# Kernel optimization log

Measured on AMD Instinct MI355X. Metric: run time of the kernel, lower is better.

The kernel has to match this reference:

```python
import jax, jax.numpy as jnp
import numpy as np

# Config (matches init_kwargs)
B, T_IN, N, F_IN = 64, 12, 500, 2
N_RES, N_DIL, N_SKIP, N_END = 64, 64, 256, 512
K_SIZE, N_BLOCKS, N_LAYERS = 2, 4, 2
EDGE_DIM, N_PRED, N_OUT = 2, 12, 1
RECEPTIVE = N_BLOCKS * (K_SIZE - 1) * (2 ** N_LAYERS - 1) + 1  # 13
DILS = [2 ** i for _ in range(N_BLOCKS) for i in range(N_LAYERS)]  # [1,2,1,2,1,2,1,2]
L = len(DILS)
BN_EPS = 1e-5


def setup_inputs() -> dict:
    key = jax.random.key(0)
    ks = jax.random.split(key, 20)
    inputs = jax.random.normal(ks[0], (B, T_IN, N, F_IN), dtype=jnp.float32)
    u = jax.random.uniform(ks[1], (EDGE_DIM, N, N), dtype=jnp.float32)
    supports = u / u.sum(-1, keepdims=True)  # row-stochastic diffusion matrices
    def w(k, shape, fan_in):
        return jax.random.normal(k, shape, dtype=jnp.float32) * (1.0 / np.sqrt(fan_in))
    return {
        "inputs": inputs,
        "supports": supports,
        "enter_w": w(ks[2], (N_RES, F_IN), F_IN),
        "enter_b": jnp.zeros((N_RES,), jnp.float32),
        "filter_w": w(ks[3], (L, N_DIL, N_RES, 1, K_SIZE), N_RES * K_SIZE),
        "filter_b": jnp.zeros((L, N_DIL), jnp.float32),
        "gate_w": w(ks[4], (L, N_DIL, N_RES, 1, K_SIZE), N_RES * K_SIZE),
        "gate_b": jnp.zeros((L, N_DIL), jnp.float32),
        "gconv_w": w(ks[5], (L, N_RES, EDGE_DIM * N_DIL), EDGE_DIM * N_DIL),
        "gconv_b": jnp.zeros((L, N_RES), jnp.float32),
        "skip_w": w(ks[6], (L, N_SKIP, N_DIL), N_DIL),
        "skip_b": jnp.zeros((L, N_SKIP), jnp.float32),
        "bn_gamma": jnp.ones((L, N_RES), jnp.float32),
        "bn_beta": jnp.zeros((L, N_RES), jnp.float32),
        "out1_w": w(ks[7], (N_END, N_SKIP), N_SKIP),
        "out1_b": jnp.zeros((N_END,), jnp.float32),
        "out2_w": w(ks[8], (N_PRED * N_OUT, N_END), N_END),
        "out2_b": jnp.zeros((N_PRED * N_OUT,), jnp.float32),
    }


def _conv_t(x, w, b, dil):
    # x: [B,C,N,T], w: [O,I,1,k] dilated along time, VALID padding
    y = jax.lax.conv_general_dilated(x, w, window_strides=(1, 1), padding="VALID",
                                     rhs_dilation=(1, dil),
                                     dimension_numbers=("NCHW", "OIHW", "NCHW"))
    return y + b[None, :, None, None]


def _forward(inputs, supports, enter_w, enter_b, filter_w, filter_b, gate_w, gate_b,
             gconv_w, gconv_b, skip_w, skip_b, bn_gamma, bn_beta,
             out1_w, out1_b, out2_w, out2_b):
    x = jnp.transpose(inputs, (0, 3, 2, 1))  # [B,F,N,T]
    pad = RECEPTIVE - x.shape[3]
    if pad > 0:
        x = jnp.pad(x, ((0, 0), (0, 0), (0, 0), (pad, 0)))
    x = jnp.einsum("of,bfnt->bont", enter_w, x) + enter_b[None, :, None, None]
    b = x.shape[0]
    skip = jnp.zeros((b, N_SKIP, N, x.shape[3]), jnp.float32)
    for i, d in enumerate(DILS):
        residual = x
        f = jnp.tanh(_conv_t(residual, filter_w[i], filter_b[i], d))
        g = jax.nn.sigmoid(_conv_t(residual, gate_w[i], gate_b[i], d))
        x = f * g  # [B, n_dil, N, t']
        s = jnp.einsum("oc,bcnt->bont", skip_w[i], x) + skip_b[i][None, :, None, None]
        skip = skip[..., -s.shape[3]:] + s
        # graph diffusion conv: propagate over each support, mix channels
        h = jnp.einsum("knm,bcmt->bkcnt", supports, x)
        bb, kk, cc, nn, tt = h.shape
        h = h.reshape(bb, kk * cc, nn, tt)
        x = jnp.einsum("oi,bint->bont", gconv_w[i], h) + gconv_b[i][None, :, None, None]
        # dropout is identity in eval mode
        x = x + residual[..., -x.shape[3]:]
        # BatchNorm2d (training-mode batch statistics)
        mean = x.mean(axis=(0, 2, 3), keepdims=True)
        var = ((x - mean) ** 2).mean(axis=(0, 2, 3), keepdims=True)
        x = (x - mean) * jax.lax.rsqrt(var + BN_EPS)
        x = x * bn_gamma[i][None, :, None, None] + bn_beta[i][None, :, None, None]
    y = jax.nn.relu(skip)  # [B, n_skips, N, 1]
    y = jax.nn.relu(jnp.einsum("os,bsnt->bont", out1_w, y) + out1_b[None, :, None, None])
    y = jnp.einsum("oe,bent->bont", out2_w, y) + out2_b[None, :, None, None]
    # [B, n_pred*n_out, N, 1] -> [B, n_pred, N, n_out]
    y = y.reshape(b, N_PRED, -1, N)
    return jnp.swapaxes(y, -1, -2)


def reference(inputs, supports, enter_w, enter_b, filter_w, filter_b, gate_w, gate_b,
              gconv_w, gconv_b, skip_w, skip_b, bn_gamma, bn_beta,
              out1_w, out1_b, out2_w, out2_b):
    return _forward(inputs, supports, enter_w, enter_b, filter_w, filter_b, gate_w, gate_b,
                    gconv_w, gconv_b, skip_w, skip_b, bn_gamma, bn_beta,
                    out1_w, out1_b, out2_w, out2_b)
```

## Files before the change

### kernel.cpp

```cpp
#include <hip/hip_runtime.h>

typedef float v4 __attribute__((ext_vector_type(4)));
typedef short bf8 __attribute__((ext_vector_type(8)));
typedef unsigned short u16;
typedef unsigned int u32;

#define DEVI __device__ __forceinline__

namespace {

constexpr int B = 64, C = 64, NPT = 500, NP = 512, T0 = 13, SC = 256, EC = 512, PR = 12;
constexpr size_t SLOTP = (size_t)B * C * NP;

constexpr size_t SZ_BUF  = 13 * SLOTP * 2;
constexpr size_t OFF_SK  = 2 * SZ_BUF;
constexpr size_t SZ_SK   = (size_t)SC * B * NPT * 4;
constexpr size_t OFF_ST  = OFF_SK + SZ_SK;
constexpr size_t OFF_STP = OFF_ST + 1024;
constexpr size_t OFF_W1T = OFF_STP + 1024;
constexpr size_t OFF_WMX = OFF_W1T + (size_t)131072*4;
constexpr size_t OFF_WFB = OFF_WMX + (size_t)65536*2;
constexpr size_t OFF_WGB = OFF_WFB + (size_t)65536*2;
constexpr size_t OFF_SWB = OFF_WGB + (size_t)65536*2;
constexpr size_t OFF_SPD = OFF_SWB + (size_t)131072*2;
constexpr size_t WS_NEED = OFF_SPD + (size_t)524288*2;

DEVI float sigm(float x) { return 1.f / (1.f + expf(-x)); }
DEVI float bf2f(u16 u) { u32 x = ((u32)u) << 16; float f; __builtin_memcpy(&f, &x, 4); return f; }
DEVI u16 f2bf(float f) { u32 x; __builtin_memcpy(&x, &f, 4); return (u16)((x + 0x7FFF + ((x >> 16) & 1)) >> 16); }
DEVI int swzA(int n, int k) { int byte = (n << 8) + (k << 1); byte ^= (((n >> 1) ^ (n >> 3)) & 7) << 4; return byte; }
DEVI int swzS(int n, int cp) { int byte = (n << 7) + (cp << 1); byte ^= (((n >> 1) ^ (n >> 3)) & 7) << 4; return byte; }

__global__ void k_debug_ws(float* __restrict__ out, float val) {
  int i = blockIdx.x * 256 + threadIdx.x;
  if (i < B * PR * NPT) out[i] = val;
}

__global__ void k_prep(const float* __restrict__ fw, const float* __restrict__ gw,
                       const float* __restrict__ sw, const float* __restrict__ gcw,
                       const float* __restrict__ o1w, const float* __restrict__ sup,
                       u16* __restrict__ WFB, u16* __restrict__ WGB,
                       u16* __restrict__ SWB, u16* __restrict__ WMX,
                       float* __restrict__ W1T, u16* __restrict__ SPD,
                       float* __restrict__ STP, double* __restrict__ ST) {
  int i = blockIdx.x * 256 + threadIdx.x;
  if (i < 65536) {
    int k = i & 127, cp = (i >> 7) & 63, l = i >> 13;
    int tap = k >> 6, c = k & 63;
    int g = ((l * 64 + cp) * 64 + c) * 2 + tap;
    WFB[i] = f2bf(fw[g]);
    WGB[i] = f2bf(gw[g]);
  }
  int j = i - 65536;
  if (j >= 0 && j < 131072) {
    int c = j & 63, o = (j >> 6) & 255, l = j >> 14;
    SWB[j] = f2bf(sw[(l * 256 + o) * 64 + c]);
  }
  int k2 = i - 196608;
  if (k2 >= 0 && k2 < 65536) WMX[k2] = f2bf(gcw[k2]);
  int m = i - 262144;
  if (m >= 0 && m < 131072) {
    int e = m & 511, o = m >> 9;
    W1T[m] = o1w[e * 256 + o];
  }
  int sp = i - 393216;
  if (sp >= 0 && sp < 524288) {
    int mm = sp & 511, n = (sp >> 9) & 511, s = sp >> 18;
    float v = (n < NPT && mm < NPT) ? sup[(size_t)s * NPT * NPT + (size_t)n * NPT + mm] : 0.f;
    SPD[sp] = f2bf(v);
  }
  int q = i - 917504;
  if (q >= 0 && q < 192) STP[q] = (q >= 64 && q < 128) ? 1.f : 0.f;
  int z = i - 917696;
  if (z >= 0 && z < 128) ST[z] = 0.0;
}

__global__ void k_enter(const float* __restrict__ in, const float* __restrict__ ew,
                        const float* __restrict__ eb, u16* __restrict__ X) {
  size_t idx = (size_t)blockIdx.x * 256 + threadIdx.x;
  if (idx >= 13 * SLOTP) return;
  int t = (int)(idx / SLOTP);
  size_t r = idx % SLOTP;
  int n = (int)(r % NP);
  int c = (int)((r / NP) % C);
  int b = (int)(r / ((size_t)NP * C));
  float v = 0.f;
  if (n < NPT) {
    v = eb[c];
    if (t > 0) {
      const float* ip = in + (((size_t)b * 12 + (t - 1)) * NPT + n) * 2;
      v += ew[c * 2] * ip[0] + ew[c * 2 + 1] * ip[1];
    }
  }
  X[idx] = f2bf(v);
}

__global__ void k_zero_sk(float* __restrict__ p) {
  size_t i = ((size_t)blockIdx.x * 256 + threadIdx.x) * 4;
  v4 z = {};
  *(v4*)&p[i] = z;
}

__global__ __launch_bounds__(512) void k_gatedconv(
    const u16* __restrict__ X, u16* __restrict__ XA,
    const float* __restrict__ STP,
    const u16* __restrict__ WFl, const float* __restrict__ bfb,
    const u16* __restrict__ WGl, const float* __restrict__ bgb,
    const u16* __restrict__ SWl, const float* __restrict__ sb,
    float* __restrict__ SK, int d, int Tp) {
  __shared__ u16 L[65536];
  const int lane = threadIdx.x, w = threadIdx.y;
  const int tid = w * 64 + lane;
  const int t = blockIdx.x, b = blockIdx.y;
  const int lrow = lane & 15, kgrp = lane >> 4;
  const int nbase = w * 64;

  for (int i = tid; i < 8192; i += 512) {
    int tap = i >> 12;
    int c = (i >> 6) & 63;
    int n0 = (i & 63) * 8;
    const u16* src = &X[(size_t)(t + tap * d) * SLOTP + ((size_t)b * C + c) * NP + n0];
    float mean = STP[c], scl = STP[64 + c], sh = STP[128 + c];
    ushort4 a = *(const ushort4*)src;
    ushort4 a2 = *(const ushort4*)(src + 4);
    u16 vals[8] = {a.x, a.y, a.z, a.w, a2.x, a2.y, a2.z, a2.w};
    int k = tap * 64 + c;
#pragma unroll
    for (int jj = 0; jj < 8; ++jj) {
      int n = n0 + jj;
      L[swzA(n, k) >> 1] = f2bf((bf2f(vals[jj]) - mean) * scl + sh);
    }
  }
  __syncthreads();

  v4 af[4][4], ag[4][4];
#pragma unroll
  for (int a1 = 0; a1 < 4; ++a1)
#pragma unroll
    for (int a2 = 0; a2 < 4; ++a2) { af[a1][a2] = (v4){0.f,0.f,0.f,0.f}; ag[a1][a2] = (v4){0.f,0.f,0.f,0.f}; }

#pragma unroll
  for (int k0 = 0; k0 < 128; k0 += 32) {
    const int kof = k0 + kgrp * 8;
    bf8 Av[4];
#pragma unroll
    for (int nt = 0; nt < 4; ++nt) {
      int n = nbase + nt * 16 + lrow;
      Av[nt] = *(const bf8*)&L[swzA(n, kof) >> 1];
    }
#pragma unroll
    for (int ct = 0; ct < 4; ++ct) {
      bf8 Fw = *(const bf8*)&WFl[(size_t)(ct * 16 + lrow) * 128 + kof];
      bf8 Gw = *(const bf8*)&WGl[(size_t)(ct * 16 + lrow) * 128 + kof];
#pragma unroll
      for (int nt = 0; nt < 4; ++nt) {
        af[nt][ct] = __builtin_amdgcn_mfma_f32_16x16x32_bf16(Av[nt], Fw, af[nt][ct], 0, 0, 0);
        ag[nt][ct] = __builtin_amdgcn_mfma_f32_16x16x32_bf16(Av[nt], Gw, ag[nt][ct], 0, 0, 0);
      }
    }
  }

  const size_t xab = (size_t)t * SLOTP + (size_t)b * C * NP;
  ushort4 ovv[4][4];
#pragma unroll
  for (int nt = 0; nt < 4; ++nt) {
    int n0s = nbase + nt * 16 + kgrp * 4;
#pragma unroll
    for (int ct = 0; ct < 4; ++ct) {
      int cp = ct * 16 + lrow;
      float fb = bfb[cp], gb2 = bgb[cp];
      ushort4 ov;
      ov.x = f2bf(tanhf(af[nt][ct][0] + fb) * sigm(ag[nt][ct][0] + gb2));
      ov.y = f2bf(tanhf(af[nt][ct][1] + fb) * sigm(ag[nt][ct][1] + gb2));
      ov.z = f2bf(tanhf(af[nt][ct][2] + fb) * sigm(ag[nt][ct][2] + gb2));
      ov.w = f2bf(tanhf(af[nt][ct][3] + fb) * sigm(ag[nt][ct][3] + gb2));
      ovv[nt][ct] = ov;
      if (n0s < NPT) *(ushort4*)&XA[xab + (size_t)cp * NP + n0s] = ov;
    }
  }

  if (t == Tp - 1) {
    __syncthreads();
#pragma unroll
    for (int nt = 0; nt < 4; ++nt) {
      int n0s = nbase + nt * 16 + kgrp * 4;
#pragma unroll
      for (int ct = 0; ct < 4; ++ct) {
        int cp = ct * 16 + lrow;
        ushort4 ov = ovv[nt][ct];
        L[swzS(n0s + 0, cp) >> 1] = ov.x;
        L[swzS(n0s + 1, cp) >> 1] = ov.y;
        L[swzS(n0s + 2, cp) >> 1] = ov.z;
        L[swzS(n0s + 3, cp) >> 1] = ov.w;
      }
    }
    __syncthreads();
#pragma unroll 1
    for (int ot = 0; ot < 16; ++ot) {
      v4 a[4];
#pragma unroll
      for (int nt = 0; nt < 4; ++nt) a[nt] = (v4){0.f,0.f,0.f,0.f};
#pragma unroll
      for (int k0 = 0; k0 < 64; k0 += 32) {
        const int kof = k0 + kgrp * 8;
        bf8 Bs = *(const bf8*)&SWl[(size_t)(ot * 16 + lrow) * 64 + kof];
#pragma unroll
        for (int nt = 0; nt < 4; ++nt) {
          int n = nbase + nt * 16 + lrow;
          bf8 Av2 = *(const bf8*)&L[swzS(n, kof) >> 1];
          a[nt] = __builtin_amdgcn_mfma_f32_16x16x32_bf16(Av2, Bs, a[nt], 0, 0, 0);
        }
      }
      int o = ot * 16 + lrow;
      float bb = sb[o];
#pragma unroll
      for (int nt = 0; nt < 4; ++nt) {
        int n0s = nbase + nt * 16 + kgrp * 4;
        if (n0s < NPT) {
          float* dst = &SK[(size_t)o * (B * NPT) + (size_t)b * NPT + n0s];
          v4 old = *(const v4*)dst;
          *(v4*)dst = old + a[nt] + bb;
        }
      }
    }
  }
}

__global__ __launch_bounds__(512) void k_diffmix(
    const u16* __restrict__ XA, const u16* __restrict__ XIN, u16* __restrict__ XOUT,
    const u16* __restrict__ SPD, const u16* __restrict__ WMXl,
    const float* __restrict__ gb, const float* __restrict__ STP, int d) {
  __shared__ u16 G[512 * 128];
  const int lane = threadIdx.x;
  const int w = threadIdx.y;
  const int t = blockIdx.x, b = blockIdx.y;
  const int lrow = lane & 15;
  const int kgrp = lane >> 4;
  const int nbase = w * 64;
  const size_t xabase = ((size_t)t * (B * C) + (size_t)b * C) * NP;

#pragma unroll 1
  for (int s = 0; s < 2; ++s) {
    v4 acc[4][4];
#pragma unroll
    for (int a = 0; a < 4; ++a)
#pragma unroll
      for (int c2 = 0; c2 < 4; ++c2) acc[a][c2] = (v4){0.f, 0.f, 0.f, 0.f};
    const u16* Sb = SPD + (size_t)s * (512 * 512);
#pragma unroll 2
    for (int k0 = 0; k0 < 512; k0 += 32) {
      const int kof = k0 + kgrp * 8;
      bf8 Af[4], Bf[4];
#pragma unroll
      for (int nt = 0; nt < 4; ++nt)
        Af[nt] = *(const bf8*)&Sb[(size_t)(nbase + nt * 16 + lrow) * 512 + kof];
#pragma unroll
      for (int ct = 0; ct < 4; ++ct)
        Bf[ct] = *(const bf8*)&XA[xabase + (size_t)(ct * 16 + lrow) * NP + kof];
#pragma unroll
      for (int nt = 0; nt < 4; ++nt)
#pragma unroll
        for (int ct = 0; ct < 4; ++ct)
          acc[nt][ct] = __builtin_amdgcn_mfma_f32_16x16x32_bf16(Af[nt], Bf[ct], acc[nt][ct], 0, 0, 0);
    }
#pragma unroll
    for (int nt = 0; nt < 4; ++nt)
#pragma unroll
      for (int ct = 0; ct < 4; ++ct)
#pragma unroll
        for (int r = 0; r < 4; ++r) {
          int n = nbase + nt * 16 + kgrp * 4 + r;
          int k = s * 64 + ct * 16 + lrow;
          int byte = (n << 8) + (k << 1);
          byte ^= (n & 7) << 4;
          G[byte >> 1] = f2bf(acc[nt][ct][r]);
        }
  }
  __syncthreads();
  v4 acc2[4][4];
#pragma unroll
  for (int a = 0; a < 4; ++a)
#pragma unroll
    for (int c2 = 0; c2 < 4; ++c2) acc2[a][c2] = (v4){0.f, 0.f, 0.f, 0.f};
#pragma unroll
  for (int k0 = 0; k0 < 128; k0 += 32) {
    const int kof = k0 + kgrp * 8;
    bf8 Af[4], Bf[4];
#pragma unroll
    for (int nt = 0; nt < 4; ++nt) {
      int n = nbase + nt * 16 + lrow;
      int byte = (n << 8) + (kof << 1);
      byte ^= (n & 7) << 4;
      Af[nt] = *(const bf8*)&G[byte >> 1];
    }
#pragma unroll
    for (int ot = 0; ot < 4; ++ot)
      Bf[ot] = *(const bf8*)&WMXl[(size_t)(ot * 16 + lrow) * 128 + kof];
#pragma unroll
    for (int nt = 0; nt < 4; ++nt)
#pragma unroll
      for (int ot = 0; ot < 4; ++ot)
        acc2[nt][ot] = __builtin_amdgcn_mfma_f32_16x16x32_bf16(Af[nt], Bf[ot], acc2[nt][ot], 0, 0, 0);
  }
  const size_t rbase = ((size_t)(t + d) * (B * C) + (size_t)b * C) * NP;
#pragma unroll
  for (int nt = 0; nt < 4; ++nt) {
    int n0 = nbase + nt * 16 + kgrp * 4;
    if (n0 >= NPT) continue;
#pragma unroll
    for (int ot = 0; ot < 4; ++ot) {
      int o = ot * 16 + lrow;
      float bias = gb[o];
      float m = STP[o], s2 = STP[64 + o], h = STP[128 + o];
      ushort4 rv = *(const ushort4*)&XIN[rbase + (size_t)o * NP + n0];
      ushort4 ov;
      ov.x = f2bf(acc2[nt][ot][0] + bias + (bf2f(rv.x) - m) * s2 + h);
      ov.y = f2bf(acc2[nt][ot][1] + bias + (bf2f(rv.y) - m) * s2 + h);
      ov.z = f2bf(acc2[nt][ot][2] + bias + (bf2f(rv.z) - m) * s2 + h);
      ov.w = f2bf(acc2[nt][ot][3] + bias + (bf2f(rv.w) - m) * s2 + h);
      *(ushort4*)&XOUT[xabase + (size_t)o * NP + n0] = ov;
    }
  }
}

__global__ void k_bnstats(const u16* __restrict__ X, double* __restrict__ st, int Tp) {
  int c = blockIdx.y;
  int perv = Tp * B * 125;
  double s = 0.0, ss = 0.0;
  for (int p = blockIdx.x * 256 + threadIdx.x; p < perv; p += 8 * 256) {
    int t = p / (B * 125);
    int r = p - t * (B * 125);
    int b = r / 125, nv = r - b * 125;
    ushort4 u = *(const ushort4*)&X[(size_t)t * SLOTP + ((size_t)b * C + c) * NP + nv * 4];
    double x0 = (double)bf2f(u.x), x1 = (double)bf2f(u.y);
    double x2 = (double)bf2f(u.z), x3 = (double)bf2f(u.w);
    s += (x0 + x1) + (x2 + x3);
    ss += (x0 * x0 + x1 * x1) + (x2 * x2 + x3 * x3);
  }
  for (int off = 32; off; off >>= 1) {
    s += __shfl_down(s, off, 64);
    ss += __shfl_down(ss, off, 64);
  }
  if ((threadIdx.x & 63) == 0) {
    atomicAdd(&st[c], s);
    atomicAdd(&st[C + c], ss);
  }
}

__global__ void k_bnfin(double* __restrict__ st, float* __restrict__ stp,
                        const float* __restrict__ gamma, const float* __restrict__ beta, int Tp) {
  int c = threadIdx.x;
  if (c < C) {
    double cnt = (double)Tp * (double)(B * NPT);
    double m = st[c] / cnt;
    double v = st[C + c] / cnt - m * m;
    stp[c] = (float)m;
    stp[C + c] = gamma[c] * rsqrtf((float)v + 1e-5f);
    stp[2 * C + c] = beta[c];
    st[c] = 0.0;
    st[C + c] = 0.0;
  }
}

__global__ __launch_bounds__(256) void k_out1(const float* __restrict__ SK,
                                              const float* __restrict__ W1T,
                                              const float* __restrict__ b1,
                                              u16* __restrict__ H1) {
  __shared__ __align__(16) float ssm[32 * 64];
  __shared__ __align__(16) float wsm[32 * 64];
  const int tx = threadIdx.x, ty = threadIdx.y;
  const int tid = ty * 16 + tx;
  const int p0 = blockIdx.x * 64, e0 = blockIdx.y * 64;
  v4 acc[4] = {};
  for (int o0 = 0; o0 < SC; o0 += 32) {
    __syncthreads();
    for (int i = tid; i < 2048; i += 256) {
      int pp = i & 63, kk = i >> 6;
      ssm[i] = fmaxf(SK[(size_t)(o0 + kk) * (B * NPT) + p0 + pp], 0.f);
      wsm[i] = W1T[(size_t)(o0 + kk) * 512 + e0 + pp];
    }
    __syncthreads();
#pragma unroll
    for (int kk = 0; kk < 32; ++kk) {
      v4 sv = *(const v4*)&ssm[kk * 64 + tx * 4];
      v4 wv = *(const v4*)&wsm[kk * 64 + ty * 4];
#pragma unroll
      for (int r = 0; r < 4; ++r) acc[r] += wv[r] * sv;
    }
  }
#pragma unroll
  for (int r = 0; r < 4; ++r) {
    int e = e0 + ty * 4 + r;
    float bb = b1[e];
    size_t ob = (size_t)e * (B * NPT) + p0 + tx * 4;
#pragma unroll
    for (int q = 0; q < 4; ++q) H1[ob + q] = f2bf(fmaxf(acc[r][q] + bb, 0.f));
  }
}

__global__ __launch_bounds__(256) void k_out2(const u16* __restrict__ H1,
                                              const float* __restrict__ W2,
                                              const float* __restrict__ b2,
                                              float* __restrict__ out) {
  int idx = blockIdx.x * 256 + threadIdx.x;
  if (idx >= B * PR * NPT) return;
  int n = idx % NPT;
  int p12 = (idx / NPT) % PR;
  int b = idx / (NPT * PR);
  size_t p = (size_t)b * NPT + n;
  const float* w = W2 + p12 * EC;
  float acc = b2[p12];
  for (int e = 0; e < EC; e += 4) {
    acc += w[e] * bf2f(H1[(size_t)e * (B * NPT) + p])
         + w[e + 1] * bf2f(H1[(size_t)(e + 1) * (B * NPT) + p])
         + w[e + 2] * bf2f(H1[(size_t)(e + 2) * (B * NPT) + p])
         + w[e + 3] * bf2f(H1[(size_t)(e + 3) * (B * NPT) + p]);
  }
  out[idx] = acc;
}

}

extern "C" void kernel_launch(void* const* d_in, const int* in_sizes, int n_in,
                              void* d_out, int out_size, void* d_ws, size_t ws_size,
                              hipStream_t stream) {
  const float* inputs  = (const float*)d_in[0];
  const float* sup     = (const float*)d_in[1];
  const float* enter_w = (const float*)d_in[2];
  const float* enter_b = (const float*)d_in[3];
  const float* filt_w  = (const float*)d_in[4];
  const float* filt_b  = (const float*)d_in[5];
  const float* gate_w  = (const float*)d_in[6];
  const float* gate_b  = (const float*)d_in[7];
  const float* gconv_w = (const float*)d_in[8];
  const float* gconv_b = (const float*)d_in[9];
  const float* skip_w  = (const float*)d_in[10];
  const float* skip_b  = (const float*)d_in[11];
  const float* bn_g    = (const float*)d_in[12];
  const float* bn_b    = (const float*)d_in[13];
  const float* o1w     = (const float*)d_in[14];
  const float* o1b     = (const float*)d_in[15];
  const float* o2w     = (const float*)d_in[16];
  const float* o2b     = (const float*)d_in[17];
  (void)in_sizes; (void)n_in; (void)out_size;

  if (ws_size < WS_NEED) {
    k_debug_ws<<<1500, 256, 0, stream>>>((float*)d_out, (float)(ws_size >> 20));
    return;
  }

  char* base = (char*)d_ws;
  u16*    buf0 = (u16*)base;
  u16*    buf1 = (u16*)(base + SZ_BUF);
  float*  SK   = (float*)(base + OFF_SK);
  double* ST   = (double*)(base + OFF_ST);
  float*  STP  = (float*)(base + OFF_STP);
  float*  W1T  = (float*)(base + OFF_W1T);
  u16*    WMX  = (u16*)(base + OFF_WMX);
  u16*    WFB  = (u16*)(base + OFF_WFB);
  u16*    WGB  = (u16*)(base + OFF_WGB);
  u16*    SWB  = (u16*)(base + OFF_SWB);
  u16*    SPD  = (u16*)(base + OFF_SPD);

  k_prep<<<3586, 256, 0, stream>>>(filt_w, gate_w, skip_w, gconv_w, o1w, sup,
                                   WFB, WGB, SWB, WMX, W1T, SPD, STP, ST);
  k_enter<<<(int)((13 * SLOTP) / 256), 256, 0, stream>>>(inputs, enter_w, enter_b, buf0);
  k_zero_sk<<<8000, 256, 0, stream>>>(SK);

  static const int dils[8] = {1, 2, 1, 2, 1, 2, 1, 2};
  u16* bufs[2] = {buf0, buf1};
  int T = T0;
  for (int l = 0; l < 8; ++l) {
    const int d = dils[l];
    const int Tp = T - d;
    u16* XIN = bufs[l & 1];
    u16* XAb = bufs[(l + 1) & 1];
    k_gatedconv<<<dim3(Tp, B), dim3(64, 8), 0, stream>>>(
        XIN, XAb, STP, WFB + l * 8192, filt_b + l * 64, WGB + l * 8192, gate_b + l * 64,
        SWB + l * 16384, skip_b + l * 256, SK, d, Tp);
    if (l < 7) {
      k_diffmix<<<dim3(Tp, B), dim3(64, 8), 0, stream>>>(
          XAb, XIN, XAb, SPD, WMX + l * 8192, gconv_b + l * 64, STP, d);
      k_bnstats<<<dim3(8, C), 256, 0, stream>>>(XAb, ST, Tp);
      k_bnfin<<<1, 64, 0, stream>>>(ST, STP, bn_g + l * 64, bn_b + l * 64, Tp);
    }
    T = Tp;
  }

  u16* H1 = buf1;
  k_out1<<<dim3(500, 8), dim3(16, 16), 0, stream>>>(SK, W1T, o1b, H1);
  k_out2<<<1500, 256, 0, stream>>>(H1, o2w, o2b, (float*)d_out);
}
```

Before: 2.313 ms.

## Fuse BatchNorm statistics into diffusion-mix epilogue via per-block partial sums

New measurement: 3.134 ms. 35.5% more time.

```diff
diff --git a/kernel.cpp b/kernel.cpp
--- a/kernel.cpp
+++ b/kernel.cpp
@@ -23,7 +23,8 @@
 constexpr size_t OFF_WGB = OFF_WFB + (size_t)65536*2;
 constexpr size_t OFF_SWB = OFF_WGB + (size_t)65536*2;
 constexpr size_t OFF_SPD = OFF_SWB + (size_t)131072*2;
-constexpr size_t WS_NEED = OFF_SPD + (size_t)524288*2;
+constexpr size_t OFF_PSUM = OFF_SPD + (size_t)524288*2;
+constexpr size_t WS_NEED = OFF_PSUM + (size_t)768*128*4;
 
 DEVI float sigm(float x) { return 1.f / (1.f + expf(-x)); }
 DEVI float bf2f(u16 u) { u32 x = ((u32)u) << 16; float f; __builtin_memcpy(&f, &x, 4); return f; }
@@ -42,7 +43,7 @@
                        u16* __restrict__ WFB, u16* __restrict__ WGB,
                        u16* __restrict__ SWB, u16* __restrict__ WMX,
                        float* __restrict__ W1T, u16* __restrict__ SPD,
-                       float* __restrict__ STP, double* __restrict__ ST) {
+                       float* __restrict__ STP) {
   int i = blockIdx.x * 256 + threadIdx.x;
   if (i < 65536) {
     int k = i & 127, cp = (i >> 7) & 63, l = i >> 13;
@@ -71,8 +72,6 @@
   }
   int q = i - 917504;
   if (q >= 0 && q < 192) STP[q] = (q >= 64 && q < 128) ? 1.f : 0.f;
-  int z = i - 917696;
-  if (z >= 0 && z < 128) ST[z] = 0.0;
 }
 
 __global__ void k_enter(const float* __restrict__ in, const float* __restrict__ ew,
@@ -229,15 +228,19 @@
 __global__ __launch_bounds__(512) void k_diffmix(
     const u16* __restrict__ XA, const u16* __restrict__ XIN, u16* __restrict__ XOUT,
     const u16* __restrict__ SPD, const u16* __restrict__ WMXl,
-    const float* __restrict__ gb, const float* __restrict__ STP, int d) {
+    const float* __restrict__ gb, const float* __restrict__ STP,
+    float* __restrict__ PSUM, int d) {
   __shared__ u16 G[512 * 128];
+  __shared__ float sst[128];
   const int lane = threadIdx.x;
   const int w = threadIdx.y;
+  const int tid = w * 64 + lane;
   const int t = blockIdx.x, b = blockIdx.y;
   const int lrow = lane & 15;
   const int kgrp = lane >> 4;
   const int nbase = w * 64;
   const size_t xabase = ((size_t)t * (B * C) + (size_t)b * C) * NP;
+  if (tid < 128) sst[tid] = 0.f;
 
 #pragma unroll 1
   for (int s = 0; s < 2; ++s) {
@@ -302,63 +305,83 @@
       for (int ot = 0; ot < 4; ++ot)
         acc2[nt][ot] = __builtin_amdgcn_mfma_f32_16x16x32_bf16(Af[nt], Bf[ot], acc2[nt][ot], 0, 0, 0);
   }
-  const size_t rbase = ((size_t)(t + d) * (B * C) + (size_t)b * C) * NP;
+
+  __syncthreads();
 #pragma unroll
   for (int nt = 0; nt < 4; ++nt) {
     int n0 = nbase + nt * 16 + kgrp * 4;
-    if (n0 >= NPT) continue;
 #pragma unroll
     for (int ot = 0; ot < 4; ++ot) {
       int o = ot * 16 + lrow;
-      float bias = gb[o];
-      float m = STP[o], s2 = STP[64 + o], h = STP[128 + o];
-      ushort4 rv = *(const ushort4*)&XIN[rbase + (size_t)o * NP + n0];
-      ushort4 ov;
-      ov.x = f2bf(acc2[nt][ot][0] + bias + (bf2f(rv.x) - m) * s2 + h);
-      ov.y = f2bf(acc2[nt][ot][1] + bias + (bf2f(rv.y) - m) * s2 + h);
-      ov.z = f2bf(acc2[nt][ot][2] + bias + (bf2f(rv.z) - m) * s2 + h);
-      ov.w = f2bf(acc2[nt][ot][3] + bias + (bf2f(rv.w) - m) * s2 + h);
-      *(ushort4*)&XOUT[xabase + (size_t)o * NP + n0] = ov;
-    }
-  }
-}
-
-__global__ void k_bnstats(const u16* __restrict__ X, double* __restrict__ st, int Tp) {
-  int c = blockIdx.y;
-  int perv = Tp * B * 125;
-  double s = 0.0, ss = 0.0;
-  for (int p = blockIdx.x * 256 + threadIdx.x; p < perv; p += 8 * 256) {
-    int t = p / (B * 125);
-    int r = p - t * (B * 125);
-    int b = r / 125, nv = r - b * 125;
-    ushort4 u = *(const ushort4*)&X[(size_t)t * SLOTP + ((size_t)b * C + c) * NP + nv * 4];
-    double x0 = (double)bf2f(u.x), x1 = (double)bf2f(u.y);
-    double x2 = (double)bf2f(u.z), x3 = (double)bf2f(u.w);
-    s += (x0 + x1) + (x2 + x3);
-    ss += (x0 * x0 + x1 * x1) + (x2 * x2 + x3 * x3);
-  }
-  for (int off = 32; off; off >>= 1) {
-    s += __shfl_down(s, off, 64);
-    ss += __shfl_down(ss, off, 64);
-  }
-  if ((threadIdx.x & 63) == 0) {
-    atomicAdd(&st[c], s);
-    atomicAdd(&st[C + c], ss);
-  }
-}
-
-__global__ void k_bnfin(double* __restrict__ st, float* __restrict__ stp,
-                        const float* __restrict__ gamma, const float* __restrict__ beta, int Tp) {
+      int byte = (o << 10) + (n0 << 1);
+      byte ^= (o & 7) << 4;
+      ushort4 gv;
+      gv.x = f2bf(acc2[nt][ot][0]);
+      gv.y = f2bf(acc2[nt][ot][1]);
+      gv.z = f2bf(acc2[nt][ot][2]);
+      gv.w = f2bf(acc2[nt][ot][3]);
+      *(ushort4*)&G[byte >> 1] = gv;
+    }
+  }
+  __syncthreads();
+  const size_t rbase = ((size_t)(t + d) * (B * C) + (size_t)b * C) * NP;
+#pragma unroll 1
+  for (int i = 0; i < 8; ++i) {
+    int idx = i * 512 + tid;
+    int o = idx >> 6;
+    int ck = idx & 63;
+    int byte = (o << 10) + (ck << 4);
+    byte ^= (o & 7) << 4;
+    ushort4 g0 = *(const ushort4*)&G[byte >> 1];
+    ushort4 g1 = *(const ushort4*)&G[(byte >> 1) + 4];
+    int n0 = ck * 8;
+    const u16* rp = &XIN[rbase + (size_t)o * NP + n0];
+    ushort4 r0 = *(const ushort4*)rp;
+    ushort4 r1 = *(const ushort4*)(rp + 4);
+    float m = STP[o], sc = STP[64 + o], h = STP[128 + o];
+    float bias = gb[o];
+    float v[8];
+    v[0] = bf2f(g0.x) + bias + (bf2f(r0.x) - m) * sc + h;
+    v[1] = bf2f(g0.y) + bias + (bf2f(r0.y) - m) * sc + h;
+    v[2] = bf2f(g0.z) + bias + (bf2f(r0.z) - m) * sc + h;
+    v[3] = bf2f(g0.w) + bias + (bf2f(r0.w) - m) * sc + h;
+    v[4] = bf2f(g1.x) + bias + (bf2f(r1.x) - m) * sc + h;
+    v[5] = bf2f(g1.y) + bias + (bf2f(r1.y) - m) * sc + h;
+    v[6] = bf2f(g1.z) + bias + (bf2f(r1.z) - m) * sc + h;
+    v[7] = bf2f(g1.w) + bias + (bf2f(r1.w) - m) * sc + h;
+    ushort4 s0, s1;
+    s0.x = f2bf(v[0]); s0.y = f2bf(v[1]); s0.z = f2bf(v[2]); s0.w = f2bf(v[3]);
+    s1.x = f2bf(v[4]); s1.y = f2bf(v[5]); s1.z = f2bf(v[6]); s1.w = f2bf(v[7]);
+    u16* op = &XOUT[xabase + (size_t)o * NP + n0];
+    *(ushort4*)op = s0;
+    *(ushort4*)(op + 4) = s1;
+    float ls = 0.f, lq = 0.f;
+#pragma unroll
+    for (int e = 0; e < 8; ++e)
+      if (n0 + e < NPT) { ls += v[e]; lq += v[e] * v[e]; }
+    atomicAdd(&sst[o], ls);
+    atomicAdd(&sst[64 + o], lq);
+  }
+  __syncthreads();
+  if (tid < 128) PSUM[(size_t)(blockIdx.y * gridDim.x + blockIdx.x) * 128 + tid] = sst[tid];
+}
+
+__global__ void k_bnfin(const float* __restrict__ PSUM, float* __restrict__ stp,
+                        const float* __restrict__ gamma, const float* __restrict__ beta,
+                        int nblk, int Tp) {
   int c = threadIdx.x;
   if (c < C) {
+    double s = 0.0, q = 0.0;
+    for (int r = 0; r < nblk; ++r) {
+      s += (double)PSUM[(size_t)r * 128 + c];
+      q += (double)PSUM[(size_t)r * 128 + 64 + c];
+    }
     double cnt = (double)Tp * (double)(B * NPT);
-    double m = st[c] / cnt;
-    double v = st[C + c] / cnt - m * m;
+    double m = s / cnt;
+    double v = q / cnt - m * m;
     stp[c] = (float)m;
     stp[C + c] = gamma[c] * rsqrtf((float)v + 1e-5f);
     stp[2 * C + c] = beta[c];
-    st[c] = 0.0;
-    st[C + c] = 0.0;
   }
 }
 
@@ -453,7 +476,6 @@
   u16*    buf0 = (u16*)base;
   u16*    buf1 = (u16*)(base + SZ_BUF);
   float*  SK   = (float*)(base + OFF_SK);
-  double* ST   = (double*)(base + OFF_ST);
   float*  STP  = (float*)(base + OFF_STP);
   float*  W1T  = (float*)(base + OFF_W1T);
   u16*    WMX  = (u16*)(base + OFF_WMX);
@@ -461,9 +483,10 @@
   u16*    WGB  = (u16*)(base + OFF_WGB);
   u16*    SWB  = (u16*)(base + OFF_SWB);
   u16*    SPD  = (u16*)(base + OFF_SPD);
+  float*  PSUM = (float*)(base + OFF_PSUM);
 
   k_prep<<<3586, 256, 0, stream>>>(filt_w, gate_w, skip_w, gconv_w, o1w, sup,
-                                   WFB, WGB, SWB, WMX, W1T, SPD, STP, ST);
+                                   WFB, WGB, SWB, WMX, W1T, SPD, STP);
   k_enter<<<(int)((13 * SLOTP) / 256), 256, 0, stream>>>(inputs, enter_w, enter_b, buf0);
   k_zero_sk<<<8000, 256, 0, stream>>>(SK);
 
@@ -480,9 +503,8 @@
         SWB + l * 16384, skip_b + l * 256, SK, d, Tp);
     if (l < 7) {
       k_diffmix<<<dim3(Tp, B), dim3(64, 8), 0, stream>>>(
-          XAb, XIN, XAb, SPD, WMX + l * 8192, gconv_b + l * 64, STP, d);
-      k_bnstats<<<dim3(8, C), 256, 0, stream>>>(XAb, ST, Tp);
-      k_bnfin<<<1, 64, 0, stream>>>(ST, STP, bn_g + l * 64, bn_b + l * 64, Tp);
+          XAb, XIN, XAb, SPD, WMX + l * 8192, gconv_b + l * 64, STP, PSUM, d);
+      k_bnfin<<<1, 64, 0, stream>>>(PSUM, STP, bn_g + l * 64, bn_b + l * 64, Tp * B, Tp);
     }
     T = Tp;
   }
```
